# Kernel tuning notes

Measured on AMD Instinct MI355X. Metric: run time of the kernel, lower is better.

Reference implementation:

```python
import jax, jax.numpy as jnp
import numpy as np

GAMMA = 1.05  # VoxelSampler.GAMMA


def setup_inputs() -> dict:
    key = jax.random.key(0)
    k1, k2, k3, k4, k5 = jax.random.split(key, 5)
    B, T, R, Np, F = 2, 8, 128, 32768, 5
    # point xy within pc_range, remaining features (z, intensity, ...) gaussian
    xy = jax.random.uniform(k1, (B, T, Np, 2), minval=-75.0, maxval=75.0)
    rest = jax.random.normal(k2, (B, T, Np, F - 2))
    points = jnp.concatenate([xy, rest], axis=-1)  # [B,T,Np,5]
    # rois: [cx,cy,cz, dx,dy,dz, yaw, vx,vy]
    ctr = jax.random.uniform(k3, (B, T, R, 3), minval=-75.0, maxval=75.0)
    dims = jax.random.uniform(k4, (B, T, R, 3), minval=1.0, maxval=6.0)
    yaw_vel = jax.random.normal(k5, (B, T, R, 3))
    trajectory_rois = jnp.concatenate([ctr, dims, yaw_vel], axis=-1)  # [B,T,R,9]
    return {"points": points, "trajectory_rois": trajectory_rois, "num_sample": 32}


def reference(points, trajectory_rois, num_sample):
    # points: [B,T,Np,5] (pre-partitioned per batch/frame, mirrors the
    # batch-column + timestamp masking of the torch code with static shapes)
    # trajectory_rois: [B,T,R,9]
    B, T, R, _ = trajectory_rois.shape
    Fdim = points.shape[-1]
    # speed = ||roi[..., -2:]||, per-roi gamma = clamp((1.05*(1+speed))**(t/5), max=2.5)
    speed = jnp.linalg.norm(trajectory_rois[..., 7:9], axis=-1)          # [B,T,R]
    t_idx = jnp.arange(T, dtype=points.dtype)
    gamma = jnp.minimum((GAMMA * (1.0 + speed)) ** (t_idx[None, :, None] / 5.0), 2.5)
    # cylindrical radius per roi: ||dims_xy/2|| * gamma
    radiis = jnp.linalg.norm(trajectory_rois[..., 3:5] * 0.5, axis=-1) * gamma  # [B,T,R]
    cx = trajectory_rois[..., 0]
    cy = trajectory_rois[..., 1]
    px = points[..., 0]
    py = points[..., 1]
    dx = px[:, :, None, :] - cx[..., None]   # [B,T,R,Np]
    dy = py[:, :, None, :] - cy[..., None]
    dis = jnp.sqrt(dx * dx + dy * dy)        # [B,T,R,Np]
    in_radius = (dis <= radiis[..., None]).astype(points.dtype)
    # topk over 0/1 mask: picks num_sample in-radius points (lowest indices first),
    # exactly like torch.topk(point_mask.float(), num_sample)
    vals, idx = jax.lax.top_k(in_radius, num_sample)  # [B,T,R,S]
    sampled = jnp.take_along_axis(points[:, :, None, :, :], idx[..., None], axis=3)  # [B,T,R,S,5]
    sampled = jnp.where(vals[..., None] > 0, sampled, jnp.zeros((), dtype=points.dtype))
    # stack frames -> permute(0,2,1,3,4) -> flatten(2,3): [B,R,T*S,5]
    out = jnp.transpose(sampled, (0, 2, 1, 3, 4)).reshape(B, R, T * num_sample, Fdim)
    return out
```

## Files before the change

### kernel.cpp

```cpp
#include <hip/hip_runtime.h>
#include <math.h>

#define B_   2
#define T_   8
#define R_   128
#define NP_  32768
#define F_   5
#define S_   32
#define SEG_ 2048
#define NSEG (NP_ / SEG_)
#define NBT  (B_ * T_)
#define NROW (NBT * R_)
#define RPB  16

__device__ __forceinline__ int mbcnt64(unsigned long long m) {
    return __builtin_amdgcn_mbcnt_hi((unsigned)(m >> 32),
           __builtin_amdgcn_mbcnt_lo((unsigned)m, 0u));
}

__global__ __launch_bounds__(256) void phase1_collect(
    const float* __restrict__ points,
    const float* __restrict__ rois,
    int* __restrict__ counts,
    unsigned short* __restrict__ hitidx)
{
    __shared__ float4 tile[SEG_ / 2];

    const int blk = blockIdx.x;
    const int rg  = blk % (R_ / RPB);
    const int bs  = blk / (R_ / RPB);
    const int seg = bs % NSEG;
    const int bt  = bs / NSEG;
    const int tid  = threadIdx.x;
    const int w    = tid >> 6;
    const int lane = tid & 63;

    const float4* src = (const float4*)(points + (size_t)bt * NP_ * F_)
                        + (size_t)seg * (SEG_ * F_ / 4);
    #pragma unroll
    for (int i = 0; i < 2; ++i) {
        const int g = tid + i * 256;
        const float4* s5 = src + (size_t)g * 5;
        const float4 a = s5[0], bq = s5[1], c = s5[2], d = s5[3], e = s5[4];
        tile[g * 2]     = make_float4(a.x, a.y, bq.y, bq.z);
        tile[g * 2 + 1] = make_float4(c.z, c.w, d.w, e.x);
    }

    const int row0 = bt * R_ + rg * RPB + w * 4;
    float vcx = 0.0f, vcy = 0.0f, vT = 0.0f;
    if (lane < 4) {
        const int row = row0 + lane;
        const int t   = bt % T_;
        const float* roi = rois + (size_t)row * 9;
        const float cx = roi[0], cy = roi[1];
        const float hx = roi[3] * 0.5f, hy = roi[4] * 0.5f;
        const float vx = roi[7], vy = roi[8];
        const float speed  = sqrtf(vx * vx + vy * vy);
        const float base_g = 1.05f * (1.0f + speed);
        const float expo   = (float)t / 5.0f;
        const float gamma  = fminf((float)pow((double)base_g, (double)expo), 2.5f);
        const float radius = sqrtf(hx * hx + hy * hy) * gamma;
        unsigned ut = __float_as_uint(radius * radius);
        while (sqrtf(__uint_as_float(ut)) > radius) --ut;
        while (sqrtf(__uint_as_float(ut + 1u)) <= radius) ++ut;
        vcx = cx; vcy = cy; vT = __uint_as_float(ut);
    }
    float cxs[4], cys[4], Ts[4];
    #pragma unroll
    for (int k = 0; k < 4; ++k) {
        cxs[k] = __shfl(vcx, k); cys[k] = __shfl(vcy, k); Ts[k] = __shfl(vT, k);
    }
    unsigned short* hs[4];
    int sels[4] = {0, 0, 0, 0};
    #pragma unroll
    for (int k = 0; k < 4; ++k)
        hs[k] = hitidx + ((size_t)(row0 + k) * NSEG + seg) * S_;

    __syncthreads();

    const int ibase = seg * SEG_;
    #pragma unroll 2
    for (int it = 0; it < SEG_ / 128; ++it) {
        const float4 q = tile[it * 64 + lane];
        const int idx0 = ibase + (it * 64 + lane) * 2;

        #pragma unroll
        for (int k = 0; k < 4; ++k) {
            const float ax = __fsub_rn(q.x, cxs[k]), ay = __fsub_rn(q.y, cys[k]);
            const float bx = __fsub_rn(q.z, cxs[k]), by = __fsub_rn(q.w, cys[k]);
            const float d2a = __fadd_rn(__fmul_rn(ax, ax), __fmul_rn(ay, ay));
            const float d2b = __fadd_rn(__fmul_rn(bx, bx), __fmul_rn(by, by));
            const bool p0 = (d2a <= Ts[k]), p1 = (d2b <= Ts[k]);
            const unsigned long long m0 = __ballot(p0), m1 = __ballot(p1);
            if (m0 | m1) {
                const int base = sels[k] + mbcnt64(m0) + mbcnt64(m1);
                if (p0 && base < S_) hs[k][base] = (unsigned short)idx0;
                if (p1) { const int s = base + (p0 ? 1 : 0);
                          if (s < S_) hs[k][s] = (unsigned short)(idx0 + 1); }
                sels[k] += __popcll(m0) + __popcll(m1);
            }
        }
    }
    if (lane == 0) {
        #pragma unroll
        for (int k = 0; k < 4; ++k)
            counts[(size_t)(row0 + k) * NSEG + seg] = (sels[k] < S_) ? sels[k] : S_;
    }
}

__global__ __launch_bounds__(256) void phase2_gather(
    const float* __restrict__ points,
    const int* __restrict__ counts,
    const unsigned short* __restrict__ hitidx,
    float* __restrict__ out)
{
    const int tid  = blockIdx.x * blockDim.x + threadIdx.x;
    const int slot = tid & (S_ - 1);
    const int row  = tid >> 5;
    if (row >= NROW) return;
    const int r  = row % R_;
    const int bt = row / R_;
    const int t  = bt % T_;
    const int b  = bt / T_;

    const int4* cp = (const int4*)(counts + (size_t)row * NSEG);
    const int4 q0 = cp[0], q1 = cp[1], q2 = cp[2], q3 = cp[3];
    const int cs[16] = {q0.x,q0.y,q0.z,q0.w, q1.x,q1.y,q1.z,q1.w,
                        q2.x,q2.y,q2.z,q2.w, q3.x,q3.y,q3.z,q3.w};
    int seg = -1, local = 0, acc = 0;
    #pragma unroll
    for (int s = 0; s < NSEG; ++s) {
        const int na = acc + cs[s];
        if (seg < 0 && slot < na) { seg = s; local = slot - acc; }
        acc = na;
    }
    const int total = (acc < S_) ? acc : S_;

    float* o = out + (((((size_t)b * R_ + r) * T_ + t) * S_) + slot) * F_;
    if (slot < total) {
        const int pi = hitidx[((size_t)row * NSEG + seg) * S_ + local];
        const float* p = points + ((size_t)bt * NP_ + pi) * F_;
        o[0] = p[0]; o[1] = p[1]; o[2] = p[2]; o[3] = p[3]; o[4] = p[4];
    } else {
        o[0] = 0.0f; o[1] = 0.0f; o[2] = 0.0f; o[3] = 0.0f; o[4] = 0.0f;
    }
}

extern "C" void kernel_launch(void* const* d_in, const int* in_sizes, int n_in,
                              void* d_out, int out_size, void* d_ws, size_t ws_size,
                              hipStream_t stream) {
    const float* points = (const float*)d_in[0];
    const float* rois   = (const float*)d_in[1];
    float* out = (float*)d_out;

    char* ws = (char*)d_ws;
    int* counts            = (int*)ws;
    unsigned short* hitidx = (unsigned short*)(ws + 131072);

    phase1_collect<<<NBT * NSEG * (R_ / RPB), 256, 0, stream>>>(points, rois, counts, hitidx);

    phase2_gather<<<(NROW * S_) / 256, 256, 0, stream>>>(points, counts, hitidx, out);
}
```

Before: 88.68 us.

## Precompute packed xy array and per-ROI radius thresholds in a prep kernel

Adds a prep kernel that extracts the x/y coordinates of all points into a compact float2 array and computes each ROI's center and squared-radius threshold once. The collect kernel then loads only the xy tile and reads the precomputed thresholds, instead of each of the 8 ROI-group blocks re-reading full 5-float points and redoing the pow and bisection. This cuts redundant global reads and per-block serial setup, but adds a kernel launch and an extra write and read of a 4 MB buffer.

```diff
diff --git a/kernel.cpp b/kernel.cpp
--- a/kernel.cpp
+++ b/kernel.cpp
@@ -18,9 +18,43 @@
            __builtin_amdgcn_mbcnt_lo((unsigned)m, 0u));
 }
 
-__global__ __launch_bounds__(256) void phase1_collect(
+__global__ __launch_bounds__(256) void xy_transpose_prep(
     const float* __restrict__ points,
     const float* __restrict__ rois,
+    float2* __restrict__ xy,
+    float4* __restrict__ rowc)
+{
+    const int j = blockIdx.x * blockDim.x + threadIdx.x;
+    if (j < NBT * NP_ / 4) {
+        const float4* src = (const float4*)points + (size_t)j * 5;
+        const float4 a = src[0], b = src[1], c = src[2], d = src[3], e = src[4];
+        float4* dst = (float4*)xy + (size_t)j * 2;
+        dst[0] = make_float4(a.x, a.y, b.y, b.z);
+        dst[1] = make_float4(c.z, c.w, d.w, e.x);
+    }
+    if (j < NROW) {
+        const int row = j;
+        const int bt  = row / R_;
+        const int t   = bt % T_;
+        const float* roi = rois + (size_t)row * 9;
+        const float cx = roi[0], cy = roi[1];
+        const float hx = roi[3] * 0.5f, hy = roi[4] * 0.5f;
+        const float vx = roi[7], vy = roi[8];
+        const float speed  = sqrtf(vx * vx + vy * vy);
+        const float base_g = 1.05f * (1.0f + speed);
+        const float expo   = (float)t / 5.0f;
+        const float gamma  = fminf((float)pow((double)base_g, (double)expo), 2.5f);
+        const float radius = sqrtf(hx * hx + hy * hy) * gamma;
+        unsigned ut = __float_as_uint(radius * radius);
+        while (sqrtf(__uint_as_float(ut)) > radius) --ut;
+        while (sqrtf(__uint_as_float(ut + 1u)) <= radius) ++ut;
+        rowc[row] = make_float4(cx, cy, __uint_as_float(ut), 0.0f);
+    }
+}
+
+__global__ __launch_bounds__(256) void phase1_collect(
+    const float2* __restrict__ xy,
+    const float4* __restrict__ rowc,
     int* __restrict__ counts,
     unsigned short* __restrict__ hitidx)
 {
@@ -35,47 +69,21 @@
     const int w    = tid >> 6;
     const int lane = tid & 63;
 
-    const float4* src = (const float4*)(points + (size_t)bt * NP_ * F_)
-                        + (size_t)seg * (SEG_ * F_ / 4);
+    const float4* src = (const float4*)(xy + (size_t)bt * NP_ + (size_t)seg * SEG_);
     #pragma unroll
-    for (int i = 0; i < 2; ++i) {
-        const int g = tid + i * 256;
-        const float4* s5 = src + (size_t)g * 5;
-        const float4 a = s5[0], bq = s5[1], c = s5[2], d = s5[3], e = s5[4];
-        tile[g * 2]     = make_float4(a.x, a.y, bq.y, bq.z);
-        tile[g * 2 + 1] = make_float4(c.z, c.w, d.w, e.x);
-    }
+    for (int i = 0; i < 4; ++i)
+        tile[i * 256 + tid] = src[i * 256 + tid];
 
     const int row0 = bt * R_ + rg * RPB + w * 4;
-    float vcx = 0.0f, vcy = 0.0f, vT = 0.0f;
-    if (lane < 4) {
-        const int row = row0 + lane;
-        const int t   = bt % T_;
-        const float* roi = rois + (size_t)row * 9;
-        const float cx = roi[0], cy = roi[1];
-        const float hx = roi[3] * 0.5f, hy = roi[4] * 0.5f;
-        const float vx = roi[7], vy = roi[8];
-        const float speed  = sqrtf(vx * vx + vy * vy);
-        const float base_g = 1.05f * (1.0f + speed);
-        const float expo   = (float)t / 5.0f;
-        const float gamma  = fminf((float)pow((double)base_g, (double)expo), 2.5f);
-        const float radius = sqrtf(hx * hx + hy * hy) * gamma;
-        unsigned ut = __float_as_uint(radius * radius);
-        while (sqrtf(__uint_as_float(ut)) > radius) --ut;
-        while (sqrtf(__uint_as_float(ut + 1u)) <= radius) ++ut;
-        vcx = cx; vcy = cy; vT = __uint_as_float(ut);
-    }
     float cxs[4], cys[4], Ts[4];
-    #pragma unroll
-    for (int k = 0; k < 4; ++k) {
-        cxs[k] = __shfl(vcx, k); cys[k] = __shfl(vcy, k); Ts[k] = __shfl(vT, k);
-    }
     unsigned short* hs[4];
     int sels[4] = {0, 0, 0, 0};
     #pragma unroll
-    for (int k = 0; k < 4; ++k)
+    for (int k = 0; k < 4; ++k) {
+        const float4 rc = rowc[row0 + k];
+        cxs[k] = rc.x; cys[k] = rc.y; Ts[k] = rc.z;
         hs[k] = hitidx + ((size_t)(row0 + k) * NSEG + seg) * S_;
-
+    }
     __syncthreads();
 
     const int ibase = seg * SEG_;
@@ -154,10 +162,14 @@
     float* out = (float*)d_out;
 
     char* ws = (char*)d_ws;
-    int* counts            = (int*)ws;
-    unsigned short* hitidx = (unsigned short*)(ws + 131072);
+    float2* xy             = (float2*)ws;
+    int* counts            = (int*)(ws + 4194304);
+    unsigned short* hitidx = (unsigned short*)(ws + 4194304 + 131072);
+    float4* rowc           = (float4*)(ws + 4194304 + 131072 + 2097152);
 
-    phase1_collect<<<NBT * NSEG * (R_ / RPB), 256, 0, stream>>>(points, rois, counts, hitidx);
+    xy_transpose_prep<<<(NBT * NP_ / 4 + 255) / 256, 256, 0, stream>>>(points, rois, xy, rowc);
+
+    phase1_collect<<<NBT * NSEG * (R_ / RPB), 256, 0, stream>>>(xy, rowc, counts, hitidx);
 
     phase2_gather<<<(NROW * S_) / 256, 256, 0, stream>>>(points, counts, hitidx, out);
 }
```

New measurement: 86.30 us. 2.7% less time.
